# Kernel tuning notes

Measured on AMD Instinct MI355X. Metric: run time of the kernel, lower is better.

## Reference

```python
import jax, jax.numpy as jnp
import numpy as np
from jax import lax

SQRT2 = 1.4142135623730951
SCALE_BOUND = 0.11
LIK_BOUND = 1e-9

def conv2d(x, w, b, pad):
    y = lax.conv_general_dilated(x, w, (1, 1), [(pad, pad), (pad, pad)],
                                 dimension_numbers=('NCHW', 'OIHW', 'NCHW'))
    return y + b[None, :, None, None]

def space_to_depth(x):  # pixel_unshuffle, block=2: [B,C,H,W]->[B,4C,H/2,W/2]
    B, C, H, W = x.shape
    x = x.reshape(B, C, H // 2, 2, W // 2, 2)
    return x.transpose(0, 1, 3, 5, 2, 4).reshape(B, 4 * C, H // 2, W // 2)

def lrelu(x):
    return jnp.where(x >= 0, x, 0.01 * x)

def gauss_cdf(x):
    return 0.5 * (1.0 + lax.erf(x / SQRT2))

def setup_inputs() -> dict:
    key = jax.random.key(0)
    ks = jax.random.split(key, 6)
    B, F_, P, H, W = 4, 128, 128, 256, 256
    inp = {
        'input': jax.random.normal(ks[0], (B, F_, H, W), jnp.float32) * 2.0,
        'condition': jax.random.normal(ks[1], (B, P // 4, H, W), jnp.float32),
        'lstm_w': jax.random.normal(ks[2], (4 * P, F_ + P, 3, 3), jnp.float32) * 0.02,
        'lstm_b': jnp.zeros((4 * P,), jnp.float32),
        'w1': jax.random.normal(ks[3], (2 * F_, P + F_, 1, 1), jnp.float32) * 0.05,
        'b1': jnp.zeros((2 * F_,), jnp.float32),
        'w2': jax.random.normal(ks[4], (2 * F_, 2 * F_, 3, 3), jnp.float32) * 0.02,
        'b2': jnp.zeros((2 * F_,), jnp.float32),
        'w3': jax.random.normal(ks[5], (2 * F_, 2 * F_, 1, 1), jnp.float32) * 0.05,
        'b3': jnp.zeros((2 * F_,), jnp.float32),
    }
    return inp

def reference(input, condition, lstm_w, lstm_b, w1, b1, w2, b2, w3, b3):
    # quantize (round with straight-through estimator, as in trc quant)
    q = input + lax.stop_gradient(jnp.round(input) - input)
    y = space_to_depth(q)                       # [B,4F,h,w]
    groups = jnp.split(y, 4, axis=1)
    if condition.shape[-2:] == input.shape[-2:]:
        condition = space_to_depth(condition)   # [B,P,h,w]
    h = condition
    c = condition
    lls = []
    for g in range(4):
        yi = groups[g - 1] if g else jnp.zeros_like(groups[0])
        # ConvLSTM cell: single conv over [input, hidden] -> 4 gates
        gates = conv2d(jnp.concatenate([yi, h], axis=1), lstm_w, lstm_b, 1)
        i_g, f_g, o_g, g_g = jnp.split(gates, 4, axis=1)
        c = jax.nn.sigmoid(f_g) * c + jax.nn.sigmoid(i_g) * jnp.tanh(g_g)
        h = jax.nn.sigmoid(o_g) * jnp.tanh(c)
        # reparam stack -> (mean, scale) condition
        t = lrelu(conv2d(jnp.concatenate([h, yi], axis=1), w1, b1, 0))
        t = lrelu(conv2d(t, w2, b2, 1))
        cnd = conv2d(t, w3, b3, 0)
        mean, scale = jnp.split(cnd, 2, axis=1)
        scale = jnp.maximum(scale, SCALE_BOUND)
        z = groups[g]
        up = gauss_cdf((z - mean + 0.5) / scale)
        lo = gauss_cdf((z - mean - 0.5) / scale)
        lls.append(jnp.maximum(up - lo, LIK_BOUND))
    likelihood = jnp.concatenate(lls, axis=1)   # [B,4F,h,w]
    return q, likelihood
```

## Files before the change

### kernel.cpp

```cpp
#include <hip/hip_runtime.h>
#include <math.h>

typedef unsigned short u16;
typedef __attribute__((ext_vector_type(8))) short bf16x8;
typedef __attribute__((ext_vector_type(4))) float f32x4;

#define PSUB8 540800
#define TSUB8 524288

__device__ __forceinline__ u16 f2bf(float f) {
  unsigned u = __float_as_uint(f);
  unsigned r = u + 0x7fffu + ((u >> 16) & 1u);
  return (u16)(r >> 16);
}
__device__ __forceinline__ float bf2f(u16 h) {
  return __uint_as_float(((unsigned)h) << 16);
}
__device__ __forceinline__ void gl16(const u16* g, const u16* l) {
  __builtin_amdgcn_global_load_lds(
      (const __attribute__((address_space(1))) void*)g,
      (__attribute__((address_space(3))) void*)l, 16, 0, 0);
}

__global__ void quant_s2d_kernel(const float* __restrict__ inp,
                                 float* __restrict__ q,
                                 u16* __restrict__ yghi) {
  int idx = blockIdx.x * 256 + threadIdx.x;
  int ww = idx & 255;
  int hh = (idx >> 8) & 255;
  int cc = (idx >> 16) & 127;
  int b  = idx >> 23;
  float v = rintf(inp[idx]);
  q[idx] = v;
  int g = cc >> 5;
  int f = ((cc & 31) << 2) | ((hh & 1) << 1) | (ww & 1);
  int y = hh >> 1, x = ww >> 1;
  int p = (b * 130 + y + 1) * 130 + 1 + x;
  yghi[((size_t)(g * 16 + (f >> 3))) * PSUB8 + (size_t)p * 8 + (f & 7)] = f2bf(v);
}

__global__ void s2d_cond_kernel(const float* __restrict__ cond,
                                u16* __restrict__ hhi, float* __restrict__ c0) {
  int idx = blockIdx.x * 256 + threadIdx.x;
  int ww = idx & 255;
  int hh = (idx >> 8) & 255;
  int cc = (idx >> 16) & 31;
  int b  = idx >> 21;
  float v = cond[idx];
  int ch = (cc << 2) | ((hh & 1) << 1) | (ww & 1);
  int y = hh >> 1, x = ww >> 1;
  int p = (b * 130 + y + 1) * 130 + 1 + x;
  hhi[(size_t)(ch >> 3) * PSUB8 + (size_t)p * 8 + (ch & 7)] = f2bf(v);
  c0[((size_t)(b * 128 + y) * 128 + x) * 128 + ch] = v;
}

template <int TAPS, int PERM>
__global__ void build_wpack(const float* __restrict__ w, u16* __restrict__ o) {
  int idx = blockIdx.x * 256 + threadIdx.x;
  int jj = idx & 7, lane = (idx >> 3) & 63, ni = (idx >> 9) & 3, wn = (idx >> 11) & 1;
  int rest = idx >> 12;
  const int NSLAB = TAPS * 8;
  int slab = rest % NSLAB, cb = rest / NSLAB;
  int c = cb * 128 + wn * 64 + ni * 16 + (lane & 15);
  int k = slab * 32 + ((lane >> 4) << 3) + jj;
  int tap = (TAPS == 9) ? (k >> 8) : 0;
  int ci = (TAPS == 9) ? (k & 255) : k;
  int oc;
  if (PERM == 0)      oc = ((c >> 4) & 3) * 128 + (c >> 7) * 32 + ((c >> 6) & 1) * 16 + (c & 15);
  else if (PERM == 2) oc = ((c >> 4) & 1) * 128 + (c >> 7) * 64 + ((c >> 6) & 1) * 32 + ((c >> 5) & 1) * 16 + (c & 15);
  else                oc = c;
  float v = w[((size_t)(oc * 256 + ci)) * TAPS + tap];
  o[idx] = f2bf(v);
}

__global__ void make_biases(const float* __restrict__ lb, const float* __restrict__ b1,
                            const float* __restrict__ b2, const float* __restrict__ b3,
                            float* __restrict__ pl, float* __restrict__ p1,
                            float* __restrict__ p2, float* __restrict__ p3) {
  int t = blockIdx.x * 256 + threadIdx.x;
  if (t < 512) {
    int gate = (t >> 4) & 3;
    int f = (t >> 7) * 32 + ((t >> 6) & 1) * 16 + (t & 15);
    pl[t] = lb[gate * 128 + f];
  }
  if (t < 256) {
    p1[t] = b1[t];
    p2[t] = b2[t];
    int m = (t >> 4) & 1;
    int f = (t >> 7) * 64 + ((t >> 6) & 1) * 32 + ((t >> 5) & 1) * 16 + (t & 15);
    p3[t] = b3[m * 128 + f];
  }
}

template <int TAPS, int NCOL, int EPI>
__global__ __launch_bounds__(256, 4)
void conv_mfma(const u16* __restrict__ a0, const u16* __restrict__ a1,
               int RS, int PAD, int skiphalf,
               const u16* __restrict__ Wpk, const float* __restrict__ biasP,
               float* __restrict__ c_io,
               u16* __restrict__ ohi, size_t OSUB, int ORS, int OPAD,
               const u16* __restrict__ zsrc, float* __restrict__ lik, int g) {
  constexpr int NSLAB = TAPS * 8;
  constexpr int NCB = NCOL / 128;
  constexpr size_t PST = (TAPS == 1 && EPI == 2) ? (size_t)TSUB8 : (size_t)PSUB8;
  __shared__ __attribute__((aligned(16))) u16 lds[16384];
  const int tid = threadIdx.x;
  const int lane = tid & 63, wid = tid >> 6;
  const int wm = wid >> 1, wn = wid & 1;
  const int fl = lane & 15, kq = lane >> 4;

  int n = blockIdx.y * NCB + blockIdx.x;
  int w_ = n >> 9, r_ = n & 511;
  int xj = r_ & 7, tt = r_ >> 3;
  const int cb = tt & (NCB - 1);
  const int YL = 64 / NCB;
  int ystrip = w_ * (8 * YL) + xj * YL + (tt / NCB);
  const int b = ystrip >> 7, y = ystrip & 127;

  const int NS = skiphalf ? NSLAB / 2 : NSLAB;
  f32x4 acc[4][4] = {};

  auto mapslab = [&](int si) -> int {
    if (!skiphalf) return si;
    int tap = si >> 2, o = si & 3;
    return tap * 8 + (skiphalf == 1 ? 4 + o : o);
  };
  auto stage = [&](int si, int buf) {
    int s = mapslab(si);
    int dy = 0, dx = 0;
    if (TAPS == 9) { int tap = s >> 3; dy = tap / 3 - 1; dx = tap % 3 - 1; }
    int cc = s & 7;
    const u16* base = (cc < 4) ? a0 : a1;
    int origin = (b * RS + y + PAD) * RS + PAD + dy * RS + dx;
#pragma unroll
    for (int t = 0; t < 2; ++t) {
      int j = wid * 2 + t;
      const u16* src = base + (size_t)((cc & 3) * 4 + (j >> 1)) * PST
                            + (size_t)(origin + (j & 1) * 64) * 8;
      gl16(src + lane * 8, &lds[buf * 4096 + j * 512]);
    }
    const u16* wbase = Wpk + ((size_t)(cb * NSLAB + s)) * 4096;
#pragma unroll
    for (int t = 0; t < 2; ++t) {
      int j = wid * 2 + t;
      gl16(wbase + j * 512 + lane * 8, &lds[8192 + buf * 4096 + j * 512]);
    }
  };
  auto compute = [&](int buf) {
    bf16x8 Ah[4], Wf[4];
#pragma unroll
    for (int i = 0; i < 4; ++i)
      Ah[i] = *(const bf16x8*)&lds[buf * 4096 + kq * 1024 + (wm * 64 + i * 16 + fl) * 8];
#pragma unroll
    for (int i = 0; i < 4; ++i)
      Wf[i] = *(const bf16x8*)&lds[8192 + buf * 4096 + wn * 2048 + i * 512 + lane * 8];
    __builtin_amdgcn_s_setprio(1);
#pragma unroll
    for (int mi = 0; mi < 4; ++mi)
#pragma unroll
      for (int ni = 0; ni < 4; ++ni)
        acc[mi][ni] = __builtin_amdgcn_mfma_f32_16x16x32_bf16(Ah[mi], Wf[ni], acc[mi][ni], 0, 0, 0);
    __builtin_amdgcn_s_setprio(0);
  };

  stage(0, 0);
  for (int s = 0; s < NS; ++s) {
    if (s + 1 < NS) {
      stage(s + 1, (s + 1) & 1);
      asm volatile("s_waitcnt vmcnt(4)" ::: "memory");
    } else {
      asm volatile("s_waitcnt vmcnt(0)" ::: "memory");
    }
    __builtin_amdgcn_s_barrier();
    compute(s & 1);
    __builtin_amdgcn_s_barrier();
  }

  if (EPI == 0) {
    const int f = cb * 32 + wn * 16 + fl;
    float bi[4];
#pragma unroll
    for (int ni = 0; ni < 4; ++ni) bi[ni] = biasP[cb * 128 + wn * 64 + ni * 16 + fl];
#pragma unroll
    for (int mi = 0; mi < 4; ++mi)
#pragma unroll
      for (int r = 0; r < 4; ++r) {
        int x = wm * 64 + mi * 16 + kq * 4 + r;
        size_t ci = ((size_t)(b * 128 + y) * 128 + x) * 128 + f;
        float ig = 1.f / (1.f + expf(-(acc[mi][0][r] + bi[0])));
        float fg = 1.f / (1.f + expf(-(acc[mi][1][r] + bi[1])));
        float og = 1.f / (1.f + expf(-(acc[mi][2][r] + bi[2])));
        float gg = tanhf(acc[mi][3][r] + bi[3]);
        float cn = fg * c_io[ci] + ig * gg;
        c_io[ci] = cn;
        float hv = og * tanhf(cn);
        size_t hx = (size_t)((b * 130 + y + 1) * 130 + 1 + x);
        ohi[(size_t)(f >> 3) * PSUB8 + hx * 8 + (f & 7)] = f2bf(hv);
      }
  } else if (EPI == 1) {
#pragma unroll
    for (int ni = 0; ni < 4; ++ni) {
      int c = cb * 128 + wn * 64 + ni * 16 + fl;
      float bv = biasP[c];
#pragma unroll
      for (int mi = 0; mi < 4; ++mi)
#pragma unroll
        for (int r = 0; r < 4; ++r) {
          int x = wm * 64 + mi * 16 + kq * 4 + r;
          float v = acc[mi][ni][r] + bv;
          v = (v >= 0.f) ? v : 0.01f * v;
          size_t op = (size_t)((b * ORS + y + OPAD) * ORS + OPAD + x);
          ohi[(size_t)(c >> 3) * OSUB + op * 8 + (c & 7)] = f2bf(v);
        }
    }
  } else {
#pragma unroll
    for (int j = 0; j < 2; ++j) {
      int f = cb * 64 + wn * 32 + j * 16 + fl;
      float bm = biasP[cb * 128 + wn * 64 + j * 32 + fl];
      float bs = biasP[cb * 128 + wn * 64 + j * 32 + 16 + fl];
#pragma unroll
      for (int mi = 0; mi < 4; ++mi)
#pragma unroll
        for (int r = 0; r < 4; ++r) {
          int x = wm * 64 + mi * 16 + kq * 4 + r;
          float mean = acc[mi][2 * j][r] + bm;
          float sc = fmaxf(acc[mi][2 * j + 1][r] + bs, 0.11f);
          size_t zp = (size_t)((b * 130 + y + 1) * 130 + 1 + x);
          float z = bf2f(zsrc[(size_t)(f >> 3) * PSUB8 + zp * 8 + (f & 7)]);
          float is = 0.70710678118654752f / sc;
          float up = 0.5f * (1.f + erff((z - mean + 0.5f) * is));
          float lo_ = 0.5f * (1.f + erff((z - mean - 0.5f) * is));
          lik[((size_t)(b * 512 + g * 128 + f) * 128 + y) * 128 + x] = fmaxf(up - lo_, 1e-9f);
        }
    }
  }
}

extern "C" void kernel_launch(void* const* d_in, const int* in_sizes, int n_in,
                              void* d_out, int out_size, void* d_ws, size_t ws_size,
                              hipStream_t stream) {
  const float* input  = (const float*)d_in[0];
  const float* cond   = (const float*)d_in[1];
  const float* lstm_w = (const float*)d_in[2];
  const float* lstm_b = (const float*)d_in[3];
  const float* w1 = (const float*)d_in[4];
  const float* b1 = (const float*)d_in[5];
  const float* w2 = (const float*)d_in[6];
  const float* b2 = (const float*)d_in[7];
  const float* w3 = (const float*)d_in[8];
  const float* b3 = (const float*)d_in[9];

  float* q   = (float*)d_out;
  float* lik = q + 33554432;

  char* ws = (char*)d_ws;
  u16* YG    = (u16*)(ws + 0);
  u16* HAhi  = (u16*)(ws + 69222400);
  u16* HBhi  = (u16*)(ws + 86528000);
  u16* T1hi  = (u16*)(ws + 103833600);
  u16* T2hi  = (u16*)(ws + 138444800);
  float* cbuf = (float*)(ws + 171999232);
  u16* WLpk = (u16*)(ws + 205553664);
  u16* W2pk = (u16*)(ws + 207912960);
  u16* W1pk = (u16*)(ws + 209092608);
  u16* W3pk = (u16*)(ws + 209223680);
  float* PL = (float*)(ws + 209354752);
  float* P1 = PL + 512;
  float* P2 = P1 + 256;
  float* P3 = P2 + 256;

  hipMemsetAsync(ws, 0, 138444800, stream);

  quant_s2d_kernel<<<131072, 256, 0, stream>>>(input, q, YG);
  s2d_cond_kernel<<<32768, 256, 0, stream>>>(cond, HAhi, cbuf);
  build_wpack<9, 0><<<4608, 256, 0, stream>>>(lstm_w, WLpk);
  build_wpack<9, 1><<<2304, 256, 0, stream>>>(w2, W2pk);
  build_wpack<1, 1><<<256, 256, 0, stream>>>(w1, W1pk);
  build_wpack<1, 2><<<256, 256, 0, stream>>>(w3, W3pk);
  make_biases<<<2, 256, 0, stream>>>(lstm_b, b1, b2, b3, PL, P1, P2, P3);

  for (int g = 0; g < 4; ++g) {
    u16* hinhi  = (g & 1) ? HBhi : HAhi;
    u16* houthi = (g & 1) ? HAhi : HBhi;
    const u16* yihi = g ? (YG + (size_t)(g - 1) * 16 * PSUB8) : hinhi;
    const u16* zg = YG + (size_t)g * 16 * PSUB8;

    conv_mfma<9, 512, 0><<<dim3(4, 512), 256, 0, stream>>>(
        yihi, hinhi, 130, 1, g ? 0 : 1,
        WLpk, PL, cbuf, houthi, PSUB8, 0, 0, nullptr, nullptr, g);
    conv_mfma<1, 256, 1><<<dim3(2, 512), 256, 0, stream>>>(
        houthi, yihi, 130, 1, g ? 0 : 2,
        W1pk, P1, nullptr, T1hi, PSUB8, 130, 1, nullptr, nullptr, g);
    conv_mfma<9, 256, 1><<<dim3(2, 512), 256, 0, stream>>>(
        T1hi, T1hi + (size_t)16 * PSUB8, 130, 1, 0,
        W2pk, P2, nullptr, T2hi, TSUB8, 128, 0, nullptr, nullptr, g);
    conv_mfma<1, 256, 2><<<dim3(2, 512), 256, 0, stream>>>(
        T2hi, T2hi + (size_t)16 * TSUB8, 128, 0, 0,
        W3pk, P3, nullptr, nullptr, 0, 0, 0, zg, lik, g);
  }
}
```

Baseline: 1.326 ms.

## Zero only halos, specialize conv template, unroll K loop, use fast transcendentals

```diff
diff --git a/kernel.cpp b/kernel.cpp
--- a/kernel.cpp
+++ b/kernel.cpp
@@ -20,6 +20,14 @@
   __builtin_amdgcn_global_load_lds(
       (const __attribute__((address_space(1))) void*)g,
       (__attribute__((address_space(3))) void*)l, 16, 0, 0);
+}
+__device__ __forceinline__ float sigm_f(float x) {
+  return __builtin_amdgcn_rcpf(1.f + __expf(-x));
+}
+__device__ __forceinline__ float tanh_f(float x) {
+  float xc = fminf(fmaxf(x, -20.f), 20.f);
+  float e = __expf(2.f * xc);
+  return (e - 1.f) * __builtin_amdgcn_rcpf(e + 1.f);
 }
 
 __global__ void quant_s2d_kernel(const float* __restrict__ inp,
@@ -52,6 +60,20 @@
   int p = (b * 130 + y + 1) * 130 + 1 + x;
   hhi[(size_t)(ch >> 3) * PSUB8 + (size_t)p * 8 + (ch & 7)] = f2bf(v);
   c0[((size_t)(b * 128 + y) * 128 + x) * 128 + ch] = v;
+}
+
+__global__ void zero_halos(u16* __restrict__ base) {
+  int e = blockIdx.x * 256 + threadIdx.x;
+  if (e >= 516 * 8) return;
+  int pb = blockIdx.y;
+  int px = e >> 3, ch = e & 7;
+  int y, x;
+  if (px < 130)      { y = 0;            x = px; }
+  else if (px < 260) { y = 129;          x = px - 130; }
+  else if (px < 388) { y = px - 260 + 1; x = 0; }
+  else               { y = px - 388 + 1; x = 129; }
+  int plane = pb >> 2, b = pb & 3;
+  base[(size_t)plane * PSUB8 + (size_t)((b * 130 + y) * 130 + x) * 8 + ch] = 0;
 }
 
 template <int TAPS, int PERM>
@@ -92,17 +114,20 @@
   }
 }
 
-template <int TAPS, int NCOL, int EPI>
+template <int TAPS, int NCOL, int EPI, int SKIP>
 __global__ __launch_bounds__(256, 4)
 void conv_mfma(const u16* __restrict__ a0, const u16* __restrict__ a1,
-               int RS, int PAD, int skiphalf,
                const u16* __restrict__ Wpk, const float* __restrict__ biasP,
                float* __restrict__ c_io,
                u16* __restrict__ ohi, size_t OSUB, int ORS, int OPAD,
                const u16* __restrict__ zsrc, float* __restrict__ lik, int g) {
   constexpr int NSLAB = TAPS * 8;
+  constexpr int NS = SKIP ? NSLAB / 2 : NSLAB;
   constexpr int NCB = NCOL / 128;
-  constexpr size_t PST = (TAPS == 1 && EPI == 2) ? (size_t)TSUB8 : (size_t)PSUB8;
+  constexpr bool COMPACT = (EPI == 2);
+  constexpr int RS = COMPACT ? 128 : 130;
+  constexpr int PAD = COMPACT ? 0 : 1;
+  constexpr size_t PST = COMPACT ? (size_t)TSUB8 : (size_t)PSUB8;
   __shared__ __attribute__((aligned(16))) u16 lds[16384];
   const int tid = threadIdx.x;
   const int lane = tid & 63, wid = tid >> 6;
@@ -117,34 +142,34 @@
   int ystrip = w_ * (8 * YL) + xj * YL + (tt / NCB);
   const int b = ystrip >> 7, y = ystrip & 127;
 
-  const int NS = skiphalf ? NSLAB / 2 : NSLAB;
   f32x4 acc[4][4] = {};
 
-  auto mapslab = [&](int si) -> int {
-    if (!skiphalf) return si;
-    int tap = si >> 2, o = si & 3;
-    return tap * 8 + (skiphalf == 1 ? 4 + o : o);
-  };
+  const int origin0 = (b * RS + y + PAD) * RS + PAD;
+  const u16* a0w = a0 + (size_t)origin0 * 8 + (size_t)wid * PST;
+  const u16* a1w = a1 + (size_t)origin0 * 8 + (size_t)wid * PST;
+  const u16* Ww  = Wpk + (size_t)cb * NSLAB * 4096 + (size_t)wid * 1024 + (size_t)lane * 8;
+  u16* ldsA = &lds[wid * 1024];
+  u16* ldsW = &lds[8192 + wid * 1024];
+
   auto stage = [&](int si, int buf) {
-    int s = mapslab(si);
-    int dy = 0, dx = 0;
-    if (TAPS == 9) { int tap = s >> 3; dy = tap / 3 - 1; dx = tap % 3 - 1; }
-    int cc = s & 7;
-    const u16* base = (cc < 4) ? a0 : a1;
-    int origin = (b * RS + y + PAD) * RS + PAD + dy * RS + dx;
-#pragma unroll
-    for (int t = 0; t < 2; ++t) {
-      int j = wid * 2 + t;
-      const u16* src = base + (size_t)((cc & 3) * 4 + (j >> 1)) * PST
-                            + (size_t)(origin + (j & 1) * 64) * 8;
-      gl16(src + lane * 8, &lds[buf * 4096 + j * 512]);
-    }
-    const u16* wbase = Wpk + ((size_t)(cb * NSLAB + s)) * 4096;
-#pragma unroll
-    for (int t = 0; t < 2; ++t) {
-      int j = wid * 2 + t;
-      gl16(wbase + j * 512 + lane * 8, &lds[8192 + buf * 4096 + j * 512]);
-    }
+    int ms;
+    if (SKIP == 0) ms = si;
+    else {
+      int tp = si >> 2, o = si & 3;
+      ms = tp * 8 + (SKIP == 1 ? 4 + o : o);
+    }
+    int cc = ms & 7;
+    int tap = ms >> 3;
+    int dy = (TAPS == 9) ? tap / 3 - 1 : 0;
+    int dx = (TAPS == 9) ? tap % 3 - 1 : 0;
+    const u16* aw = (cc < 4) ? a0w : a1w;
+    long abase = (long)(cc & 3) * 4 * (long)PST + (long)(dy * RS + dx) * 8;
+#pragma unroll
+    for (int t = 0; t < 2; ++t)
+      gl16(aw + abase + t * 512 + lane * 8, ldsA + buf * 4096 + t * 512);
+#pragma unroll
+    for (int t = 0; t < 2; ++t)
+      gl16(Ww + (long)ms * 4096 + t * 512, ldsW + buf * 4096 + t * 512);
   };
   auto compute = [&](int buf) {
     bf16x8 Ah[4], Wf[4];
@@ -164,6 +189,7 @@
   };
 
   stage(0, 0);
+#pragma unroll
   for (int s = 0; s < NS; ++s) {
     if (s + 1 < NS) {
       stage(s + 1, (s + 1) & 1);
@@ -187,13 +213,13 @@
       for (int r = 0; r < 4; ++r) {
         int x = wm * 64 + mi * 16 + kq * 4 + r;
         size_t ci = ((size_t)(b * 128 + y) * 128 + x) * 128 + f;
-        float ig = 1.f / (1.f + expf(-(acc[mi][0][r] + bi[0])));
-        float fg = 1.f / (1.f + expf(-(acc[mi][1][r] + bi[1])));
-        float og = 1.f / (1.f + expf(-(acc[mi][2][r] + bi[2])));
-        float gg = tanhf(acc[mi][3][r] + bi[3]);
+        float ig = sigm_f(acc[mi][0][r] + bi[0]);
+        float fg = sigm_f(acc[mi][1][r] + bi[1]);
+        float og = sigm_f(acc[mi][2][r] + bi[2]);
+        float gg = tanh_f(acc[mi][3][r] + bi[3]);
         float cn = fg * c_io[ci] + ig * gg;
         c_io[ci] = cn;
-        float hv = og * tanhf(cn);
+        float hv = og * tanh_f(cn);
         size_t hx = (size_t)((b * 130 + y + 1) * 130 + 1 + x);
         ohi[(size_t)(f >> 3) * PSUB8 + hx * 8 + (f & 7)] = f2bf(hv);
       }
@@ -270,7 +296,7 @@
   float* P2 = P1 + 256;
   float* P3 = P2 + 256;
 
-  hipMemsetAsync(ws, 0, 138444800, stream);
+  zero_halos<<<dim3(17, 512), 256, 0, stream>>>((u16*)ws);
 
   quant_s2d_kernel<<<131072, 256, 0, stream>>>(input, q, YG);
   s2d_cond_kernel<<<32768, 256, 0, stream>>>(cond, HAhi, cbuf);
@@ -286,17 +312,22 @@
     const u16* yihi = g ? (YG + (size_t)(g - 1) * 16 * PSUB8) : hinhi;
     const u16* zg = YG + (size_t)g * 16 * PSUB8;
 
-    conv_mfma<9, 512, 0><<<dim3(4, 512), 256, 0, stream>>>(
-        yihi, hinhi, 130, 1, g ? 0 : 1,
-        WLpk, PL, cbuf, houthi, PSUB8, 0, 0, nullptr, nullptr, g);
-    conv_mfma<1, 256, 1><<<dim3(2, 512), 256, 0, stream>>>(
-        houthi, yihi, 130, 1, g ? 0 : 2,
-        W1pk, P1, nullptr, T1hi, PSUB8, 130, 1, nullptr, nullptr, g);
-    conv_mfma<9, 256, 1><<<dim3(2, 512), 256, 0, stream>>>(
-        T1hi, T1hi + (size_t)16 * PSUB8, 130, 1, 0,
-        W2pk, P2, nullptr, T2hi, TSUB8, 128, 0, nullptr, nullptr, g);
-    conv_mfma<1, 256, 2><<<dim3(2, 512), 256, 0, stream>>>(
-        T2hi, T2hi + (size_t)16 * TSUB8, 128, 0, 0,
-        W3pk, P3, nullptr, nullptr, 0, 0, 0, zg, lik, g);
-  }
-}
+    if (g == 0) {
+      conv_mfma<9, 512, 0, 1><<<dim3(4, 512), 256, 0, stream>>>(
+          hinhi, hinhi, WLpk, PL, cbuf, houthi, PSUB8, 0, 0, nullptr, nullptr, g);
+      conv_mfma<1, 256, 1, 2><<<dim3(2, 512), 256, 0, stream>>>(
+          houthi, houthi, W1pk, P1, nullptr, T1hi, PSUB8, 130, 1, nullptr, nullptr, g);
+    } else {
+      conv_mfma<9, 512, 0, 0><<<dim3(4, 512), 256, 0, stream>>>(
+          yihi, hinhi, WLpk, PL, cbuf, houthi, PSUB8, 0, 0, nullptr, nullptr, g);
+      conv_mfma<1, 256, 1, 0><<<dim3(2, 512), 256, 0, stream>>>(
+          houthi, yihi, W1pk, P1, nullptr, T1hi, PSUB8, 130, 1, nullptr, nullptr, g);
+    }
+    conv_mfma<9, 256, 1, 0><<<dim3(2, 512), 256, 0, stream>>>(
+        T1hi, T1hi + (size_t)16 * PSUB8, W2pk, P2, nullptr, T2hi, TSUB8, 128, 0,
+        nullptr, nullptr, g);
+    conv_mfma<1, 256, 2, 0><<<dim3(2, 512), 256, 0, stream>>>(
+        T2hi, T2hi + (size_t)16 * TSUB8, W3pk, P3, nullptr, nullptr, 0, 0, 0,
+        zg, lik, g);
+  }
+}
```

Measured after the change: 1.179 ms. 11.1% less time.
